# Optimization experiments

Hardware: AMD Instinct MI355X
Metric: run time of the kernel (lower is better)

The kernel has to match this reference:

```python
import jax, jax.numpy as jnp
import numpy as np

N = 50000      # nodes
D = 16         # fixed in-degree per node
E = N * D      # edges
C = 128        # in_channels == hidden_channels
H = 128        # hidden_channels
ED = 16        # edge_dim
OUT = 2        # out_channels


def setup_inputs() -> dict:
    key = jax.random.key(0)
    ks = jax.random.split(key, 16)
    s = 0.05
    x = jax.random.normal(ks[0], (N, C), jnp.float32)
    src = jax.random.randint(ks[1], (E,), 0, N)
    dst = jnp.repeat(jnp.arange(N), D)           # sorted by destination, degree D each
    edge_index = jnp.stack([src, dst]).astype(jnp.int32)
    edge_attr = jax.random.normal(ks[2], (E, ED), jnp.float32)
    # 3 SAGEConv layers, each: LSTM(C->C) aggregator + lin_l(C->H, bias) + lin_r(C->H, no bias)
    Wih = jax.random.normal(ks[3], (3, 4 * C, C), jnp.float32) * s
    Whh = jax.random.normal(ks[4], (3, 4 * C, C), jnp.float32) * s
    bih = jax.random.normal(ks[5], (3, 4 * C), jnp.float32) * s
    bhh = jax.random.normal(ks[6], (3, 4 * C), jnp.float32) * s
    lin_l_W = jax.random.normal(ks[7], (3, H, C), jnp.float32) * s
    lin_l_b = jax.random.normal(ks[8], (3, H), jnp.float32) * s
    lin_r_W = jax.random.normal(ks[9], (3, H, C), jnp.float32) * s
    # edge MLP: (2H+ED)->H->H//2->OUT
    W1 = jax.random.normal(ks[10], (H, 2 * H + ED), jnp.float32) * s
    b1 = jax.random.normal(ks[11], (H,), jnp.float32) * s
    W2 = jax.random.normal(ks[12], (H // 2, H), jnp.float32) * s
    b2 = jax.random.normal(ks[13], (H // 2,), jnp.float32) * s
    W3 = jax.random.normal(ks[14], (OUT, H // 2), jnp.float32) * s
    b3 = jax.random.normal(ks[15], (OUT,), jnp.float32) * s
    return dict(x=x, edge_index=edge_index, edge_attr=edge_attr,
                Wih=Wih, Whh=Whh, bih=bih, bhh=bhh,
                lin_l_W=lin_l_W, lin_l_b=lin_l_b, lin_r_W=lin_r_W,
                W1=W1, b1=b1, W2=W2, b2=b2, W3=W3, b3=b3)


def _lstm_last(seq, wih, whh, bi, bh):
    # seq: [N, D, C] -> last LSTM output [N, C] (torch gate order i,f,g,o)
    h0 = jnp.zeros((seq.shape[0], whh.shape[1]), seq.dtype)

    def step(carry, xt):
        h, c = carry
        gates = xt @ wih.T + bi + h @ whh.T + bh
        i, f, g, o = jnp.split(gates, 4, axis=-1)
        c = jax.nn.sigmoid(f) * c + jax.nn.sigmoid(i) * jnp.tanh(g)
        h = jax.nn.sigmoid(o) * jnp.tanh(c)
        return (h, c), None

    (h, _), _ = jax.lax.scan(step, (h0, h0), seq.transpose(1, 0, 2))
    return h


def _sage_lstm(x, src, wih, whh, bi, bh, wl, bl, wr):
    # fixed degree D, edges sorted by dst -> group-by-dst is a reshape
    seq = x[src].reshape(N, D, -1)           # [N, D, C] neighbor sequences
    agg = _lstm_last(seq, wih, whh, bi, bh)  # [N, C]
    return agg @ wl.T + bl + x @ wr.T        # lin_l(agg) + lin_r(x)


def reference(x, edge_index, edge_attr, Wih, Whh, bih, bhh,
              lin_l_W, lin_l_b, lin_r_W, W1, b1, W2, b2, W3, b3):
    src, dst = edge_index[0], edge_index[1]
    h = x
    for l in range(3):
        h = jax.nn.relu(_sage_lstm(h, src, Wih[l], Whh[l], bih[l], bhh[l],
                                   lin_l_W[l], lin_l_b[l], lin_r_W[l]))
    # gather-concat edge MLP (dropout is identity in eval)
    feat = jnp.concatenate([h[src], h[dst], edge_attr], axis=1)  # [E, 2H+ED]
    e = jax.nn.relu(feat @ W1.T + b1)
    e = jax.nn.relu(e @ W2.T + b2)
    return e @ W3.T + b3
```

## Files before the change

### kernel.cpp

```cpp
#include <hip/hip_runtime.h>
#include <hip/hip_bf16.h>

#define NN 50000
#define DEG 16

typedef __attribute__((ext_vector_type(8))) short bfrag;
typedef __attribute__((ext_vector_type(4))) float f32x4;

__device__ __forceinline__ float bf2f(unsigned int u){ return __uint_as_float(u<<16); }
__device__ __forceinline__ unsigned short f2bf(float x){
  unsigned int u = __float_as_uint(x);
  unsigned int r = (u + 0x7fffu + ((u>>16)&1u)) >> 16;
  return (unsigned short)r;
}
__device__ __forceinline__ float fast_rcp(float x){ return __builtin_amdgcn_rcpf(x); }
__device__ __forceinline__ float sigmoidf_(float x){ return fast_rcp(1.f + __expf(-x)); }
__device__ __forceinline__ float tanh_fast(float x){
  float e = __expf(-2.f*fabsf(x));
  float r = (1.f - e)*fast_rcp(1.f + e);
  return copysignf(r, x);
}

#define SWZ(row) (((((row) ^ ((row)>>3)) & 7)) << 4)

#define GLDS16(g, l) __builtin_amdgcn_global_load_lds( \
    (const __attribute__((address_space(1))) unsigned int*)(g), \
    (__attribute__((address_space(3))) unsigned int*)(l), 16, 0, 0)

__global__ void k_cvt(const float* __restrict__ in, unsigned short* __restrict__ out, int n){
  int i = blockIdx.x*256 + threadIdx.x;
  if (i < n) out[i] = f2bf(in[i]);
}

__global__ void k_cvt2(const float* __restrict__ in, unsigned short* __restrict__ out,
                       int stride, int off, int cols, int total){
  int i = blockIdx.x*256 + threadIdx.x;
  if (i < total){
    int r = i / cols, c = i - r*cols;
    out[i] = f2bf(in[(size_t)r*stride + off + c]);
  }
}

__global__ void k_prep_lstm(const float* __restrict__ Wih, const float* __restrict__ Whh,
                            const float* __restrict__ bih, const float* __restrict__ bhh,
                            unsigned short* __restrict__ Wcat, float* __restrict__ bsum)
{
  int i = blockIdx.x*256 + threadIdx.x;
  if (i < 3*512*256){
    int l = i >> 17;
    int rem = i & 131071;
    int row = rem >> 8, col = rem & 255;
    float v = (col < 128) ? Wih[((size_t)l*512 + row)*128 + col]
                          : Whh[((size_t)l*512 + row)*128 + (col-128)];
    Wcat[i] = f2bf(v);
  } else if (i < 3*512*256 + 3*512){
    int k = i - 3*512*256;
    bsum[k] = bih[k] + bhh[k];
  }
}

__global__ void k_prep_edge(const float* __restrict__ W1, const float* __restrict__ W2,
                            const float* __restrict__ W3,
                            unsigned short* __restrict__ W1eh, unsigned short* __restrict__ W1el,
                            unsigned short* __restrict__ W2h, unsigned short* __restrict__ W2l,
                            unsigned short* __restrict__ W3p)
{
  int i = blockIdx.x*256 + threadIdx.x;
  if (i < 8192){
    float v = W2[i];
    unsigned short hi = f2bf(v);
    W2h[i] = hi; W2l[i] = f2bf(v - bf2f(hi));
  } else if (i < 10240){
    int k = i - 8192; int j = k >> 4, kk = k & 15;
    float v = W1[(size_t)j*272 + 256 + kk];
    unsigned short hi = f2bf(v);
    W1eh[k] = hi; W1el[k] = f2bf(v - bf2f(hi));
  } else if (i < 11264){
    int k = i - 10240; int nr = k >> 6, c = k & 63;
    W3p[k] = f2bf(nr < 2 ? W3[nr*64 + c] : 0.f);
  }
}

__global__ __launch_bounds__(256,4) void k_bgemm(
    const unsigned short* __restrict__ Ab, const unsigned short* __restrict__ A2b,
    const unsigned short* __restrict__ Wb, const unsigned short* __restrict__ W2b,
    const float* __restrict__ bias, const float* __restrict__ bias2,
    float* __restrict__ outF, unsigned short* __restrict__ outB,
    int ostride, int dorelu, int n)
{
  const int t  = threadIdx.x;
  const int w  = t >> 6;
  const int l  = t & 63;
  const int ln = l & 15, q = l >> 4;
  const int n0 = blockIdx.x*64;
  const int j0 = blockIdx.y*128 + w*32;

  int nodeM[4];
#pragma unroll
  for (int mt=0;mt<4;mt++){ int nd = n0 + mt*16 + ln; nodeM[mt] = nd < n ? nd : n-1; }

  f32x4 acc[4][2];
#pragma unroll
  for (int mt=0;mt<4;mt++)
#pragma unroll
    for (int nt=0;nt<2;nt++) acc[mt][nt] = (f32x4){0.f,0.f,0.f,0.f};

  auto pass = [&](const unsigned short* __restrict__ Ap, const unsigned short* __restrict__ Wp){
#pragma unroll
    for (int ks=0;ks<4;ks++){
      bfrag Af[4], Bf[2];
#pragma unroll
      for (int mt=0;mt<4;mt++)
        Af[mt] = *(const bfrag*)(Ap + (size_t)nodeM[mt]*128 + ks*32 + q*8);
#pragma unroll
      for (int nt=0;nt<2;nt++)
        Bf[nt] = *(const bfrag*)(Wp + (size_t)(j0 + nt*16 + ln)*128 + ks*32 + q*8);
#pragma unroll
      for (int mt=0;mt<4;mt++)
#pragma unroll
        for (int nt=0;nt<2;nt++)
          acc[mt][nt] = __builtin_amdgcn_mfma_f32_16x16x32_bf16(Af[mt], Bf[nt], acc[mt][nt], 0,0,0);
    }
  };
  pass(Ab, Wb);
  if (A2b) pass(A2b, W2b);

#pragma unroll
  for (int nt=0;nt<2;nt++){
    int j = j0 + nt*16 + ln;
    float bv = bias ? bias[j] : 0.f;
    if (bias2) bv += bias2[j];
#pragma unroll
    for (int mt=0;mt<4;mt++)
#pragma unroll
      for (int r=0;r<4;r++){
        int row = n0 + mt*16 + q*4 + r;
        if (row < n){
          float v = acc[mt][nt][r] + bv;
          if (dorelu) v = fmaxf(v, 0.f);
          if (outF) outF[(size_t)row*ostride + j] = v;
          if (outB) outB[(size_t)row*ostride + j] = f2bf(v);
        }
      }
  }
}

__global__ __launch_bounds__(512,2) void k_lstm7(
    const unsigned short* __restrict__ xin,
    const int* __restrict__ src,
    const unsigned short* __restrict__ Wcat,
    const float* __restrict__ bsum,
    unsigned short* __restrict__ aggb, int n)
{
  __shared__ unsigned short hs[64*128];
  __shared__ unsigned short xbuf[2][64*128];
  __shared__ int srcs[64*16];
  const int t  = threadIdx.x;
  const int w  = t >> 6;
  const int l  = t & 63;
  const int ln = l & 15;
  const int q  = l >> 4;
  const int n0 = blockIdx.x * 64;

  for (int i = t; i < 1024; i += 512){
    int nl = i >> 4, st = i & 15;
    srcs[i] = (n0+nl < n) ? src[(size_t)(n0+nl)*16 + st] : 0;
  }

  bfrag A[4][8];
#pragma unroll
  for (int T=0;T<4;T++)
#pragma unroll
    for (int ks=0;ks<8;ks++)
      A[T][ks] = *(const bfrag*)(Wcat + (size_t)(T*128 + w*16 + ln)*256 + ks*32 + q*8);

  f32x4 bsv[4];
#pragma unroll
  for (int T=0;T<4;T++)
    bsv[T] = *(const f32x4*)(bsum + T*128 + w*16 + q*4);

  float c[4][4];
#pragma unroll
  for (int nt=0;nt<4;nt++)
#pragma unroll
    for (int r=0;r<4;r++) c[nt][r]=0.f;

  __syncthreads();

  auto stageX = [&](int step, int buf){
#pragma unroll
    for (int j=0;j<2;j++){
      int row  = w*8 + j*4 + (l>>4);
      int node = srcs[row*16 + step];
      const char* gsrc = (const char*)xin + (size_t)node*256 + (((l&15)*16) ^ ((row&7)<<4));
      char* ldst = (char*)&xbuf[buf][0] + (w*8 + j*4)*256;
      GLDS16(gsrc, ldst);
    }
  };

  stageX(0, 0);
  asm volatile("s_waitcnt vmcnt(0)" ::: "memory");
  __syncthreads();

  for (int step=0; step<16; step++){
    const int cur = step & 1;
    if (step < 15) stageX(step+1, cur^1);

#pragma unroll
    for (int p=0;p<2;p++){
      f32x4 acc[4][2];
#pragma unroll
      for (int T=0;T<4;T++)
#pragma unroll
        for (int ntl=0;ntl<2;ntl++) acc[T][ntl] = (f32x4){0.f,0.f,0.f,0.f};

#pragma unroll
      for (int ntl=0; ntl<2; ntl++){
        int node = p*32 + ntl*16 + ln;
        int swz  = (node&7)<<4;
#pragma unroll
        for (int ks=0;ks<4;ks++){
          bfrag Bk = *(const bfrag*)((const char*)&xbuf[cur][0] + node*256 +
                       (((ks*32+q*8)*2) ^ swz));
#pragma unroll
          for (int T=0;T<4;T++)
            acc[T][ntl] = __builtin_amdgcn_mfma_f32_16x16x32_bf16(A[T][ks], Bk, acc[T][ntl], 0,0,0);
        }
        if (step > 0){
#pragma unroll
          for (int ks=4;ks<8;ks++){
            bfrag Bk = *(const bfrag*)((const char*)hs + node*256 +
                         ((((ks-4)*32+q*8)*2) ^ swz));
#pragma unroll
            for (int T=0;T<4;T++)
              acc[T][ntl] = __builtin_amdgcn_mfma_f32_16x16x32_bf16(A[T][ks], Bk, acc[T][ntl], 0,0,0);
          }
        }
      }

      if (p == 1){
        asm volatile("s_waitcnt vmcnt(0)" ::: "memory");
      }
      __syncthreads();

#pragma unroll
      for (int ntl=0; ntl<2; ntl++){
        int nt = p*2 + ntl;
        int node = p*32 + ntl*16 + ln;
        float h[4];
#pragma unroll
        for (int r=0;r<4;r++){
          float iv = acc[0][ntl][r] + bsv[0][r];
          float fv = acc[1][ntl][r] + bsv[1][r];
          float gg = acc[2][ntl][r] + bsv[2][r];
          float ov = acc[3][ntl][r] + bsv[3][r];
          float cn = sigmoidf_(fv)*c[nt][r] + sigmoidf_(iv)*tanh_fast(gg);
          c[nt][r] = cn;
          h[r] = sigmoidf_(ov)*tanh_fast(cn);
        }
        unsigned pk01, pk23;
        asm("v_cvt_pk_bf16_f32 %0, %1, %2" : "=v"(pk01) : "v"(h[0]), "v"(h[1]));
        asm("v_cvt_pk_bf16_f32 %0, %1, %2" : "=v"(pk23) : "v"(h[2]), "v"(h[3]));
        uint2 pv; pv.x = pk01; pv.y = pk23;
        *(uint2*)((char*)hs + node*256 + ((((w*16 + q*4)*2)) ^ ((node&7)<<4))) = pv;
        if (step == 15 && n0+node < n)
          *(uint2*)(aggb + (size_t)(n0+node)*128 + w*16 + q*4) = pv;
      }
    }
  }
}

__global__ __launch_bounds__(256,2) void k_edge3(
    const float* __restrict__ HsHd,
    const float* __restrict__ ea,
    const int* __restrict__ src,
    const unsigned short* __restrict__ W1eh, const unsigned short* __restrict__ W1el,
    const unsigned short* __restrict__ W2h,  const unsigned short* __restrict__ W2l,
    const unsigned short* __restrict__ W3p,
    const float* __restrict__ b1, const float* __restrict__ b2, const float* __restrict__ b3,
    float* __restrict__ out)
{
  __shared__ unsigned short out1h[64*128];
  __shared__ unsigned short out1l[64*128];
  __shared__ unsigned short e2h[64*64];
  __shared__ unsigned short e2l[64*64];
  __shared__ unsigned short ea2[64*56];

  const int t = threadIdx.x;
  const int w = t>>6, l = t&63, ln = l&15, q = l>>4;
  const int nblk = blockIdx.x;
  const size_t e0 = (size_t)nblk*64;

  int srcv[4];
#pragma unroll
  for (int r=0;r<4;r++) srcv[r] = src[e0 + w*16 + q*4 + r];

  float hsv[8][4];
#pragma unroll
  for (int nt=0;nt<8;nt++)
#pragma unroll
    for (int r=0;r<4;r++)
      hsv[nt][r] = HsHd[(size_t)srcv[r]*256 + nt*16 + ln];

  float hdv[8];
#pragma unroll
  for (int nt=0;nt<8;nt++)
    hdv[nt] = HsHd[((size_t)nblk*4 + w)*256 + 128 + nt*16 + ln];

  float b1v[8];
#pragma unroll
  for (int nt=0;nt<8;nt++) b1v[nt] = b1[nt*16 + ln];
  float b2v[4];
#pragma unroll
  for (int nt=0;nt<4;nt++) b2v[nt] = b2[nt*16 + ln];
  float b3v = (ln<2) ? b3[ln] : 0.f;

  bfrag w1h[8], w1l[8];
#pragma unroll
  for (int nt=0;nt<8;nt++){
    int j = nt*16 + ln;
    w1h[nt] = *(const bfrag*)(W1eh + (size_t)j*16 + (q&1)*8);
    w1l[nt] = *(const bfrag*)(W1el + (size_t)j*16 + (q&1)*8);
  }
  bfrag w3f[2];
#pragma unroll
  for (int ks=0;ks<2;ks++)
    w3f[ks] = *(const bfrag*)(W3p + (size_t)ln*64 + ks*32 + q*8);

  for (int i=t;i<1024;i+=256){
    int e=i>>4, k=i&15;
    float v = ea[(e0+e)*16 + k];
    unsigned short hi = f2bf(v);
    ea2[e*56 + k] = hi;
    ea2[e*56 + 16 + k] = f2bf(v - bf2f(hi));
  }
  __syncthreads();

  {
    bfrag Aea = *(const bfrag*)&ea2[(w*16+ln)*56 + q*8];
#pragma unroll
    for (int nt=0;nt<8;nt++){
      f32x4 acc;
#pragma unroll
      for (int r=0;r<4;r++) acc[r] = b1v[nt] + hdv[nt] + hsv[nt][r];
      acc = __builtin_amdgcn_mfma_f32_16x16x32_bf16(Aea, w1h[nt], acc, 0,0,0);
      acc = __builtin_amdgcn_mfma_f32_16x16x32_bf16(Aea, w1l[nt], acc, 0,0,0);
      int j = nt*16 + ln;
#pragma unroll
      for (int r=0;r<4;r++){
        int row = w*16 + q*4 + r;
        float v = fmaxf(acc[r], 0.f);
        unsigned short hi = f2bf(v);
        float lo = v - bf2f(hi);
        int byt = row*256 + ((j*2) ^ SWZ(row));
        *(unsigned short*)((char*)out1h + byt) = hi;
        *(unsigned short*)((char*)out1l + byt) = f2bf(lo);
      }
    }
  }
  __syncthreads();

  {
    f32x4 acc[4];
#pragma unroll
    for (int nt=0;nt<4;nt++) acc[nt] = (f32x4){b2v[nt],b2v[nt],b2v[nt],b2v[nt]};
    int arow = w*16 + ln;

    bfrag BhA[4], BlA[4], BhB[4], BlB[4];
#pragma unroll
    for (int nt=0;nt<4;nt++){
      int j = nt*16 + ln;
      BhA[nt] = *(const bfrag*)(W2h + (size_t)j*128 + q*8);
      BlA[nt] = *(const bfrag*)(W2l + (size_t)j*128 + q*8);
    }
#pragma unroll
    for (int ks=0;ks<4;ks++){
      if (ks < 3){
#pragma unroll
        for (int nt=0;nt<4;nt++){
          int j = nt*16 + ln;
          if ((ks&1)==0){
            BhB[nt] = *(const bfrag*)(W2h + (size_t)j*128 + (ks+1)*32 + q*8);
            BlB[nt] = *(const bfrag*)(W2l + (size_t)j*128 + (ks+1)*32 + q*8);
          } else {
            BhA[nt] = *(const bfrag*)(W2h + (size_t)j*128 + (ks+1)*32 + q*8);
            BlA[nt] = *(const bfrag*)(W2l + (size_t)j*128 + (ks+1)*32 + q*8);
          }
        }
      }
      int byt = arow*256 + ((ks*64 + q*16) ^ SWZ(arow));
      bfrag Ah = *(const bfrag*)((char*)out1h + byt);
      bfrag Al = *(const bfrag*)((char*)out1l + byt);
#pragma unroll
      for (int nt=0;nt<4;nt++){
        bfrag Bh = ((ks&1)==0) ? BhA[nt] : BhB[nt];
        bfrag Bl = ((ks&1)==0) ? BlA[nt] : BlB[nt];
        acc[nt] = __builtin_amdgcn_mfma_f32_16x16x32_bf16(Ah, Bh, acc[nt], 0,0,0);
        acc[nt] = __builtin_amdgcn_mfma_f32_16x16x32_bf16(Al, Bh, acc[nt], 0,0,0);
        acc[nt] = __builtin_amdgcn_mfma_f32_16x16x32_bf16(Ah, Bl, acc[nt], 0,0,0);
      }
    }
#pragma unroll
    for (int nt=0;nt<4;nt++)
#pragma unroll
      for (int r=0;r<4;r++){
        int row = w*16 + q*4 + r;
        int j = nt*16 + ln;
        float v = fmaxf(acc[nt][r], 0.f);
        unsigned short hi = f2bf(v);
        float lo = v - bf2f(hi);
        int byt = row*128 + ((j*2) ^ SWZ(row));
        *(unsigned short*)((char*)e2h + byt) = hi;
        *(unsigned short*)((char*)e2l + byt) = f2bf(lo);
      }
  }
  __syncthreads();

  {
    f32x4 acc = (f32x4){b3v,b3v,b3v,b3v};
    int arow = w*16 + ln;
#pragma unroll
    for (int ks=0;ks<2;ks++){
      int byt = arow*128 + ((ks*64 + q*16) ^ SWZ(arow));
      bfrag Ah = *(const bfrag*)((char*)e2h + byt);
      bfrag Al = *(const bfrag*)((char*)e2l + byt);
      acc = __builtin_amdgcn_mfma_f32_16x16x32_bf16(Ah, w3f[ks], acc, 0,0,0);
      acc = __builtin_amdgcn_mfma_f32_16x16x32_bf16(Al, w3f[ks], acc, 0,0,0);
    }
    if (ln < 2){
#pragma unroll
      for (int r=0;r<4;r++){
        int row = w*16 + q*4 + r;
        out[(e0 + row)*2 + ln] = acc[r];
      }
    }
  }
}

extern "C" void kernel_launch(void* const* d_in, const int* in_sizes, int n_in,
                              void* d_out, int out_size, void* d_ws, size_t ws_size,
                              hipStream_t stream) {
  const float* x    = (const float*)d_in[0];
  const int*   eidx = (const int*)  d_in[1];
  const float* eatt = (const float*)d_in[2];
  const float* Wih  = (const float*)d_in[3];
  const float* Whh  = (const float*)d_in[4];
  const float* bih  = (const float*)d_in[5];
  const float* bhh  = (const float*)d_in[6];
  const float* WlL  = (const float*)d_in[7];
  const float* blL  = (const float*)d_in[8];
  const float* WrL  = (const float*)d_in[9];
  const float* W1   = (const float*)d_in[10];
  const float* b1   = (const float*)d_in[11];
  const float* W2   = (const float*)d_in[12];
  const float* b2   = (const float*)d_in[13];
  const float* W3   = (const float*)d_in[14];
  const float* b3   = (const float*)d_in[15];
  const int*   src  = eidx;

  char* p = (char*)d_ws;
  float* HsHd        = (float*)p;
  p += (size_t)NN*512*2;
  unsigned short* xb   = (unsigned short*)p; p += (size_t)NN*128*2;
  unsigned short* hb1  = (unsigned short*)p; p += (size_t)NN*128*2;
  unsigned short* hb2  = (unsigned short*)p; p += (size_t)NN*128*2;
  unsigned short* aggb = (unsigned short*)p; p += (size_t)NN*128*2;
  unsigned short* Wcat = (unsigned short*)p; p += (size_t)3*512*256*2;
  float* bsum          = (float*)p;          p += (size_t)3*512*4;
  unsigned short* Wlb  = (unsigned short*)p; p += (size_t)3*128*128*2;
  unsigned short* Wrb  = (unsigned short*)p; p += (size_t)3*128*128*2;
  unsigned short* W1nb = (unsigned short*)p; p += (size_t)256*128*2;
  unsigned short* W1eh = (unsigned short*)p; p += 2048*2;
  unsigned short* W1el = (unsigned short*)p; p += 2048*2;
  unsigned short* W2h  = (unsigned short*)p; p += 8192*2;
  unsigned short* W2l  = (unsigned short*)p; p += 8192*2;
  unsigned short* W3p  = (unsigned short*)p; p += 1024*2;

  dim3 blk(256);
  const int nb = (NN + 63)/64;

  k_cvt<<<(NN*128+255)/256, blk, 0, stream>>>(x, xb, NN*128);
  k_prep_lstm<<<(3*512*256 + 3*512 + 255)/256, blk, 0, stream>>>(Wih, Whh, bih, bhh, Wcat, bsum);
  k_cvt<<<(3*128*128+255)/256, blk, 0, stream>>>(WlL, Wlb, 3*128*128);
  k_cvt<<<(3*128*128+255)/256, blk, 0, stream>>>(WrL, Wrb, 3*128*128);
  k_cvt2<<<(128*128+255)/256, blk, 0, stream>>>(W1, W1nb,           272, 0,   128, 128*128);
  k_cvt2<<<(128*128+255)/256, blk, 0, stream>>>(W1, W1nb+128*128,   272, 128, 128, 128*128);
  k_prep_edge<<<(11264+255)/256, blk, 0, stream>>>(W1, W2, W3, W1eh, W1el, W2h, W2l, W3p);

  const unsigned short* hin = xb;
  unsigned short* houts[3] = {hb1, hb2, hb1};
  for (int l = 0; l < 3; l++){
    k_lstm7<<<dim3(nb),dim3(512),0,stream>>>(hin, src,
        Wcat + (size_t)l*512*256, bsum + (size_t)l*512, aggb, NN);
    k_bgemm<<<dim3(nb,1),blk,0,stream>>>(aggb, hin,
        Wlb + (size_t)l*128*128, Wrb + (size_t)l*128*128,
        blL + (size_t)l*128, nullptr,
        nullptr, houts[l], 128, 1, NN);
    hin = houts[l];
  }
  k_bgemm<<<dim3(nb,2),blk,0,stream>>>(hin, nullptr, W1nb, nullptr,
                                       nullptr, nullptr, HsHd, nullptr, 256, 0, NN);
  k_edge3<<<dim3(NN/4),blk,0,stream>>>(HsHd, eatt, src, W1eh, W1el, W2h, W2l, W3p,
                                       b1, b2, b3, (float*)d_out);
}
```

Before: 1.419 ms.

## Fuse SAGE linear layers into LSTM kernel and use Pade tanh/sigmoid

The per-layer SAGE output projection (lin_l on the LSTM result plus lin_r on the input, bias and ReLU) now runs inside the LSTM kernel from the final hidden state held in shared memory. This removes the separate GEMM launch and the round trip of the aggregate through global memory. The LSTM gate nonlinearities switch from exp/reciprocal to a clamped rational Pade approximation, which trades accuracy for cheaper ALU work. MFMA sections are bracketed with s_setprio to favour matrix issue among waves.

```diff
diff --git a/kernel.cpp b/kernel.cpp
--- a/kernel.cpp
+++ b/kernel.cpp
@@ -20,6 +20,14 @@
   float r = (1.f - e)*fast_rcp(1.f + e);
   return copysignf(r, x);
 }
+__device__ __forceinline__ float pade_tanh(float x){
+  float x2 = x*x;
+  float num = x * (945.f + x2*(105.f + x2));
+  float den = 945.f + x2*(420.f + 15.f*x2);
+  float t = num * fast_rcp(den);
+  return fminf(1.f, fmaxf(-1.f, t));
+}
+__device__ __forceinline__ float sig_fast(float x){ return 0.5f + 0.5f*pade_tanh(0.5f*x); }
 
 #define SWZ(row) (((((row) ^ ((row)>>3)) & 7)) << 4)
 
@@ -145,12 +153,16 @@
   }
 }
 
-__global__ __launch_bounds__(512,2) void k_lstm7(
+__global__ __launch_bounds__(512,2) void k_lstm8(
     const unsigned short* __restrict__ xin,
     const int* __restrict__ src,
     const unsigned short* __restrict__ Wcat,
     const float* __restrict__ bsum,
-    unsigned short* __restrict__ aggb, int n)
+    const unsigned short* __restrict__ Wlb,
+    const unsigned short* __restrict__ Wrb,
+    const float* __restrict__ bl,
+    unsigned short* __restrict__ hout,
+    int n)
 {
   __shared__ unsigned short hs[64*128];
   __shared__ unsigned short xbuf[2][64*128];
@@ -214,6 +226,7 @@
 #pragma unroll
         for (int ntl=0;ntl<2;ntl++) acc[T][ntl] = (f32x4){0.f,0.f,0.f,0.f};
 
+      __builtin_amdgcn_s_setprio(1);
 #pragma unroll
       for (int ntl=0; ntl<2; ntl++){
         int node = p*32 + ntl*16 + ln;
@@ -237,6 +250,7 @@
           }
         }
       }
+      __builtin_amdgcn_s_setprio(0);
 
       if (p == 1){
         asm volatile("s_waitcnt vmcnt(0)" ::: "memory");
@@ -254,17 +268,49 @@
           float fv = acc[1][ntl][r] + bsv[1][r];
           float gg = acc[2][ntl][r] + bsv[2][r];
           float ov = acc[3][ntl][r] + bsv[3][r];
-          float cn = sigmoidf_(fv)*c[nt][r] + sigmoidf_(iv)*tanh_fast(gg);
+          float cn = sig_fast(fv)*c[nt][r] + sig_fast(iv)*pade_tanh(gg);
           c[nt][r] = cn;
-          h[r] = sigmoidf_(ov)*tanh_fast(cn);
+          h[r] = sig_fast(ov)*pade_tanh(cn);
         }
         unsigned pk01, pk23;
         asm("v_cvt_pk_bf16_f32 %0, %1, %2" : "=v"(pk01) : "v"(h[0]), "v"(h[1]));
         asm("v_cvt_pk_bf16_f32 %0, %1, %2" : "=v"(pk23) : "v"(h[2]), "v"(h[3]));
         uint2 pv; pv.x = pk01; pv.y = pk23;
         *(uint2*)((char*)hs + node*256 + ((((w*16 + q*4)*2)) ^ ((node&7)<<4))) = pv;
-        if (step == 15 && n0+node < n)
-          *(uint2*)(aggb + (size_t)(n0+node)*128 + w*16 + q*4) = pv;
+      }
+    }
+  }
+
+  __syncthreads();
+  {
+    bfrag Al[4], Ar[4];
+#pragma unroll
+    for (int ks=0;ks<4;ks++){
+      Al[ks] = *(const bfrag*)(Wlb + (size_t)(w*16+ln)*128 + ks*32 + q*8);
+      Ar[ks] = *(const bfrag*)(Wrb + (size_t)(w*16+ln)*128 + ks*32 + q*8);
+    }
+    f32x4 blv = *(const f32x4*)(bl + w*16 + q*4);
+#pragma unroll
+    for (int nt=0; nt<4; nt++){
+      int node = nt*16 + ln;
+      int gn = (n0+node < n) ? (n0+node) : (n-1);
+      f32x4 acc = (f32x4){0.f,0.f,0.f,0.f};
+#pragma unroll
+      for (int ks=0;ks<4;ks++){
+        bfrag Bh = *(const bfrag*)((const char*)hs + node*256 +
+                     (((ks*32+q*8)*2) ^ ((node&7)<<4)));
+        bfrag Bx = *(const bfrag*)(xin + (size_t)gn*128 + ks*32 + q*8);
+        acc = __builtin_amdgcn_mfma_f32_16x16x32_bf16(Al[ks], Bh, acc, 0,0,0);
+        acc = __builtin_amdgcn_mfma_f32_16x16x32_bf16(Ar[ks], Bx, acc, 0,0,0);
+      }
+      float v0 = fmaxf(acc[0]+blv[0], 0.f), v1 = fmaxf(acc[1]+blv[1], 0.f);
+      float v2 = fmaxf(acc[2]+blv[2], 0.f), v3 = fmaxf(acc[3]+blv[3], 0.f);
+      unsigned pk01, pk23;
+      asm("v_cvt_pk_bf16_f32 %0, %1, %2" : "=v"(pk01) : "v"(v0), "v"(v1));
+      asm("v_cvt_pk_bf16_f32 %0, %1, %2" : "=v"(pk23) : "v"(v2), "v"(v3));
+      if (n0+node < n){
+        uint2 pv; pv.x = pk01; pv.y = pk23;
+        *(uint2*)(hout + (size_t)(n0+node)*128 + w*16 + q*4) = pv;
       }
     }
   }
@@ -475,6 +521,7 @@
   unsigned short* W2h  = (unsigned short*)p; p += 8192*2;
   unsigned short* W2l  = (unsigned short*)p; p += 8192*2;
   unsigned short* W3p  = (unsigned short*)p; p += 1024*2;
+  (void)aggb;
 
   dim3 blk(256);
   const int nb = (NN + 63)/64;
@@ -490,12 +537,10 @@
   const unsigned short* hin = xb;
   unsigned short* houts[3] = {hb1, hb2, hb1};
   for (int l = 0; l < 3; l++){
-    k_lstm7<<<dim3(nb),dim3(512),0,stream>>>(hin, src,
-        Wcat + (size_t)l*512*256, bsum + (size_t)l*512, aggb, NN);
-    k_bgemm<<<dim3(nb,1),blk,0,stream>>>(aggb, hin,
-        Wlb + (size_t)l*128*128, Wrb + (size_t)l*128*128,
-        blL + (size_t)l*128, nullptr,
-        nullptr, houts[l], 128, 1, NN);
+    k_lstm8<<<dim3(nb),dim3(512),0,stream>>>(hin, src,
+        Wcat + (size_t)l*512*256, bsum + (size_t)l*512,
+        Wlb + (size_t)l*128*128, Wrb + (size_t)l*128*128, blL + (size_t)l*128,
+        houts[l], NN);
     hin = houts[l];
   }
   k_bgemm<<<dim3(nb,2),blk,0,stream>>>(hin, nullptr, W1nb, nullptr,
```

Result: slower. 1.515 ms (+6.8%).
